# Kernel optimization log

Measured on AMD Instinct MI355X. Metric: run time of the kernel, lower is better.

Reference implementation:

```python
import jax, jax.numpy as jnp
import numpy as np

T, I, H, O = 4096, 1024, 2048, 512


def setup_inputs() -> dict:
    key = jax.random.key(0)
    ks = jax.random.split(key, 7)
    s = 1.0 / np.sqrt(H)
    return {
        "input_seq": jax.random.normal(ks[0], (T, I), dtype=jnp.float32),
        "W_ih": jax.random.uniform(ks[1], (4 * H, I), jnp.float32, -s, s),
        "W_hh": jax.random.uniform(ks[2], (4 * H, H), jnp.float32, -s, s),
        "b_ih": jax.random.uniform(ks[3], (4 * H,), jnp.float32, -s, s),
        "b_hh": jax.random.uniform(ks[4], (4 * H,), jnp.float32, -s, s),
        "W_lin": jax.random.uniform(ks[5], (O, H), jnp.float32, -s, s),
        "b_lin": jax.random.uniform(ks[6], (O,), jnp.float32, -s, s),
    }


def reference(input_seq, W_ih, W_hh, b_ih, b_hh, W_lin, b_lin):
    # Precompute input-to-gates projection for all timesteps: [T, 4H]
    x_gates = input_seq @ W_ih.T + (b_ih + b_hh)

    def step(carry, xg):
        h, c = carry  # [H], [H]
        gates = xg + W_hh @ h  # [4H]; PyTorch gate order: i, f, g, o
        i, f, g, o = jnp.split(gates, 4)
        i = jax.nn.sigmoid(i)
        f = jax.nn.sigmoid(f)
        g = jnp.tanh(g)
        o = jax.nn.sigmoid(o)
        c = f * c + i * g
        h = o * jnp.tanh(c)
        return (h, c), None

    h0 = jnp.zeros((H,), dtype=input_seq.dtype)
    c0 = jnp.zeros((H,), dtype=input_seq.dtype)
    (h_last, _), _ = jax.lax.scan(step, (h0, c0), x_gates)
    # predictions[-1] depends only on the final hidden state
    return h_last @ W_lin.T + b_lin  # [O]
```

## Files before the change

kernel.cpp:

```cpp
#include <hip/hip_runtime.h>
#include <math.h>

#define T_SEQ 4096
#define I_DIM 1024
#define H_DIM 2048
#define O_DIM 512
#define G4    8192

__global__ __launch_bounds__(256) void gemm_xg(
    const float* __restrict__ A, const float* __restrict__ W,
    const float* __restrict__ b_ih, const float* __restrict__ b_hh,
    float* __restrict__ xg)
{
  __shared__ __align__(16) float As[16][132];
  __shared__ __align__(16) float Bs[16][132];
  const int tid = threadIdx.x;
  const int t0 = blockIdx.y * 128;
  const int r0 = blockIdx.x * 128;
  const int tx = tid & 15, ty = tid >> 4;

  float acc[8][8];
  #pragma unroll
  for (int i = 0; i < 8; ++i)
    #pragma unroll
    for (int j = 0; j < 8; ++j) acc[i][j] = 0.f;

  for (int k0 = 0; k0 < I_DIM; k0 += 16) {
    #pragma unroll
    for (int i = 0; i < 2; ++i) {
      int lin = tid + i * 256;
      int row = lin >> 2;
      int kq  = (lin & 3) << 2;
      float4 va = *(const float4*)&A[(size_t)(t0 + row) * I_DIM + k0 + kq];
      As[kq+0][row] = va.x; As[kq+1][row] = va.y; As[kq+2][row] = va.z; As[kq+3][row] = va.w;
      float4 vb = *(const float4*)&W[(size_t)(r0 + row) * I_DIM + k0 + kq];
      Bs[kq+0][row] = vb.x; Bs[kq+1][row] = vb.y; Bs[kq+2][row] = vb.z; Bs[kq+3][row] = vb.w;
    }
    __syncthreads();
    #pragma unroll
    for (int kk = 0; kk < 16; ++kk) {
      float4 a0 = *(const float4*)&As[kk][ty*8];
      float4 a1 = *(const float4*)&As[kk][ty*8+4];
      float4 b0 = *(const float4*)&Bs[kk][tx*8];
      float4 b1 = *(const float4*)&Bs[kk][tx*8+4];
      float av[8] = {a0.x,a0.y,a0.z,a0.w,a1.x,a1.y,a1.z,a1.w};
      float bv[8] = {b0.x,b0.y,b0.z,b0.w,b1.x,b1.y,b1.z,b1.w};
      #pragma unroll
      for (int i = 0; i < 8; ++i)
        #pragma unroll
        for (int j = 0; j < 8; ++j)
          acc[i][j] = fmaf(av[i], bv[j], acc[i][j]);
    }
    __syncthreads();
  }

  const int rbase = r0 + tx * 8;
  const int g = rbase >> 11;
  const int q = (rbase & 2047) >> 3;
  float bias[8];
  #pragma unroll
  for (int j = 0; j < 8; ++j) bias[j] = b_ih[rbase + j] + b_hh[rbase + j];
  #pragma unroll
  for (int i = 0; i < 8; ++i) {
    int t = t0 + ty * 8 + i;
    float* dst = &xg[(size_t)t * G4 + q * 32 + g * 8];
    float4 o0 = make_float4(acc[i][0]+bias[0], acc[i][1]+bias[1], acc[i][2]+bias[2], acc[i][3]+bias[3]);
    float4 o1 = make_float4(acc[i][4]+bias[4], acc[i][5]+bias[5], acc[i][6]+bias[6], acc[i][7]+bias[7]);
    *(float4*)&dst[0] = o0;
    *(float4*)&dst[4] = o1;
  }
}

__device__ __forceinline__ float sigf(float x) {
  return 1.f / (1.f + __expf(-x));
}
__device__ __forceinline__ float tanh_fast(float x) {
  return 1.f - 2.f / (__expf(2.f * x) + 1.f);
}

__global__ __launch_bounds__(512, 2) void lstm_seq(
    const float* __restrict__ W_hh, const float* __restrict__ xg,
    uint2* __restrict__ hbuf )
{
  __shared__ __align__(16) float smem[21000];
  float* hsh = smem;

  const int tid  = threadIdx.x;
  const int b    = blockIdx.x;
  const int lane = tid & 63;
  const int w    = tid >> 6;

  float4 wt[4][8];
  #pragma unroll
  for (int g = 0; g < 4; ++g) {
    const float* wr = &W_hh[(size_t)(g * H_DIM + 8 * b + w) * H_DIM + 4 * lane];
    #pragma unroll
    for (int k = 0; k < 8; ++k) wt[g][k] = *(const float4*)&wr[256 * k];
  }

  float c_reg = 0.f;
  bool gaveup = false;

  const float* xp0 = &xg[(size_t)0 * G4 + b * 32 + w];
  float xgi = xp0[0], xgf = xp0[8], xgg = xp0[16], xgo = xp0[24];

  for (int t = 0; t < T_SEQ; ++t) {
    const uint2* hb = hbuf + ((t & 1) << 11);
    const unsigned tag = (unsigned)t;

    const uint2* a0 = hb + 256 * w + 4 * lane;
    uint4 f0, f1;
    int tries = 0;
    for (;;) {
      asm volatile("global_load_dwordx4 %0, %2, off sc0 sc1\n\t"
                   "global_load_dwordx4 %1, %3, off sc0 sc1\n\t"
                   "s_waitcnt vmcnt(0)"
                   : "=&v"(f0), "=&v"(f1)
                   : "v"(a0), "v"(a0 + 2)
                   : "memory");
      bool ok = (f0.y == tag) & (f0.w == tag) & (f1.y == tag) & (f1.w == tag);
      if (__all(ok) || gaveup) break;
      if (++tries > (1 << 17)) { gaveup = true; break; }
    }

    float* hd = hsh + ((t & 1) << 11);
    float4 hv4 = make_float4(__uint_as_float(f0.x), __uint_as_float(f0.z),
                             __uint_as_float(f1.x), __uint_as_float(f1.z));
    *(float4*)&hd[256 * w + 4 * lane] = hv4;

    float nxi = 0.f, nxf = 0.f, nxg = 0.f, nxo = 0.f;
    if (t + 1 < T_SEQ) {
      const float* xp = &xg[(size_t)(t + 1) * G4 + b * 32 + w];
      nxi = xp[0]; nxf = xp[8]; nxg = xp[16]; nxo = xp[24];
    }

    __syncthreads();

    float s0 = 0.f, s1 = 0.f, s2 = 0.f, s3 = 0.f;
    #pragma unroll
    for (int k = 0; k < 8; ++k) {
      float4 hv = *(const float4*)&hd[4 * lane + 256 * k];
      s0 = fmaf(wt[0][k].x, hv.x, s0); s0 = fmaf(wt[0][k].y, hv.y, s0);
      s0 = fmaf(wt[0][k].z, hv.z, s0); s0 = fmaf(wt[0][k].w, hv.w, s0);
      s1 = fmaf(wt[1][k].x, hv.x, s1); s1 = fmaf(wt[1][k].y, hv.y, s1);
      s1 = fmaf(wt[1][k].z, hv.z, s1); s1 = fmaf(wt[1][k].w, hv.w, s1);
      s2 = fmaf(wt[2][k].x, hv.x, s2); s2 = fmaf(wt[2][k].y, hv.y, s2);
      s2 = fmaf(wt[2][k].z, hv.z, s2); s2 = fmaf(wt[2][k].w, hv.w, s2);
      s3 = fmaf(wt[3][k].x, hv.x, s3); s3 = fmaf(wt[3][k].y, hv.y, s3);
      s3 = fmaf(wt[3][k].z, hv.z, s3); s3 = fmaf(wt[3][k].w, hv.w, s3);
    }

    #pragma unroll
    for (int sh = 32; sh >= 1; sh >>= 1) {
      s0 += __shfl_xor(s0, sh, 64);
      s1 += __shfl_xor(s1, sh, 64);
      s2 += __shfl_xor(s2, sh, 64);
      s3 += __shfl_xor(s3, sh, 64);
    }

    if (lane == 0) {
      float iv = sigf(s0 + xgi);
      float fv = sigf(s1 + xgf);
      float gv = tanh_fast(s2 + xgg);
      float ov = sigf(s3 + xgo);
      c_reg = fv * c_reg + iv * gv;
      float hv = ov * tanh_fast(c_reg);
      uint2 pv;
      pv.x = __float_as_uint(hv);
      pv.y = (unsigned)(t + 1);
      uint2* dst = hbuf + (((t + 1) & 1) << 11) + 8 * b + w;
      asm volatile("global_store_dwordx2 %0, %1, off sc0 sc1"
                   :: "v"(dst), "v"(pv) : "memory");
    }

    xgi = nxi; xgf = nxf; xgg = nxg; xgo = nxo;
  }
}

__global__ __launch_bounds__(256) void proj_out(
    const float* __restrict__ W_lin, const float* __restrict__ b_lin,
    const uint2* __restrict__ hpairs, float* __restrict__ out)
{
  const int tid = threadIdx.x;
  const int lane = tid & 63;
  const int w4 = tid >> 6;
  const int o = blockIdx.x * 4 + w4;
  const float* wr = &W_lin[(size_t)o * H_DIM + 4 * lane];
  float s = 0.f;
  #pragma unroll
  for (int k = 0; k < 8; ++k) {
    float4 wv = *(const float4*)&wr[256 * k];
    uint4 p0 = *(const uint4*)&hpairs[4 * lane + 256 * k];
    uint4 p1 = *(const uint4*)&hpairs[4 * lane + 256 * k + 2];
    s = fmaf(wv.x, __uint_as_float(p0.x), s);
    s = fmaf(wv.y, __uint_as_float(p0.z), s);
    s = fmaf(wv.z, __uint_as_float(p1.x), s);
    s = fmaf(wv.w, __uint_as_float(p1.z), s);
  }
  #pragma unroll
  for (int sh = 32; sh >= 1; sh >>= 1) s += __shfl_xor(s, sh, 64);
  if (lane == 0) out[o] = s + b_lin[o];
}

extern "C" void kernel_launch(void* const* d_in, const int* in_sizes, int n_in,
                              void* d_out, int out_size, void* d_ws, size_t ws_size,
                              hipStream_t stream)
{
  const float* input = (const float*)d_in[0];
  const float* W_ih  = (const float*)d_in[1];
  const float* W_hh  = (const float*)d_in[2];
  const float* b_ih  = (const float*)d_in[3];
  const float* b_hh  = (const float*)d_in[4];
  const float* W_lin = (const float*)d_in[5];
  const float* b_lin = (const float*)d_in[6];
  float* out = (float*)d_out;

  char* ws = (char*)d_ws;
  const size_t XG_BYTES = (size_t)T_SEQ * G4 * sizeof(float);
  float* xg   = (float*)ws;
  uint2* hbuf = (uint2*)(ws + XG_BYTES);

  hipMemsetAsync(ws + XG_BYTES, 0, 2 * H_DIM * sizeof(uint2), stream);

  gemm_xg<<<dim3(64, 32), 256, 0, stream>>>(input, W_ih, b_ih, b_hh, xg);
  lstm_seq<<<256, 512, 0, stream>>>(W_hh, xg, hbuf);
  proj_out<<<128, 256, 0, stream>>>(W_lin, b_lin, hbuf, out);
}
```

Baseline: 13.07 ms.

## Relay hidden state through per-XCC gateway block mailboxes for L2-local polling

For each XCC, the first block to arrive becomes a gateway. It polls the global h buffer with system-coherent loads and copies what it reads into a mailbox buffer owned by that XCC. The other blocks poll the mailbox with sc0-only loads that can hit the shared L2, and fall back to the LLC path after many failed tries. The aim is to cut cross-die coherent polling traffic and latency in the per-step grid-wide synchronization. The cost is an extra relay hop through the gateway, and correctness relies on non-coherent L2 visibility of the gateway's plain stores.

```diff
diff --git a/kernel.cpp b/kernel.cpp
--- a/kernel.cpp
+++ b/kernel.cpp
@@ -80,16 +80,32 @@
 
 __global__ __launch_bounds__(512, 2) void lstm_seq(
     const float* __restrict__ W_hh, const float* __restrict__ xg,
-    uint2* __restrict__ hbuf )
+    uint2* __restrict__ hbuf ,
+    uint2* __restrict__ mail ,
+    int*   __restrict__ gwcnt )
 {
   __shared__ __align__(16) float smem[21000];
   float* hsh = smem;
+  __shared__ int s_gw;
+  __shared__ int s_xcc;
 
   const int tid  = threadIdx.x;
   const int b    = blockIdx.x;
   const int lane = tid & 63;
   const int w    = tid >> 6;
 
+  if (tid == 0) {
+    unsigned xcc;
+    asm volatile("s_getreg_b32 %0, hwreg(HW_REG_XCC_ID, 0, 32)" : "=s"(xcc));
+    xcc &= 7;
+    s_xcc = (int)xcc;
+    s_gw  = (atomicAdd(&gwcnt[xcc], 1) == 0) ? 1 : 0;
+  }
+  __syncthreads();
+  const int  xcc   = s_xcc;
+  const bool is_gw = (s_gw != 0);
+  uint2* mb_base = mail + (xcc << 12);
+
   float4 wt[4][8];
   #pragma unroll
   for (int g = 0; g < 4; ++g) {
@@ -100,30 +116,61 @@
 
   float c_reg = 0.f;
   bool gaveup = false;
+  bool use_llc = false;
 
   const float* xp0 = &xg[(size_t)0 * G4 + b * 32 + w];
   float xgi = xp0[0], xgf = xp0[8], xgg = xp0[16], xgo = xp0[24];
 
   for (int t = 0; t < T_SEQ; ++t) {
-    const uint2* hb = hbuf + ((t & 1) << 11);
+    const int par = t & 1;
     const unsigned tag = (unsigned)t;
-
-    const uint2* a0 = hb + 256 * w + 4 * lane;
+    const uint2* ha = hbuf + (par << 11) + 256 * w + 4 * lane;
+    uint2*       ma = mb_base + (par << 11) + 256 * w + 4 * lane;
+
     uint4 f0, f1;
-    int tries = 0;
-    for (;;) {
-      asm volatile("global_load_dwordx4 %0, %2, off sc0 sc1\n\t"
-                   "global_load_dwordx4 %1, %3, off sc0 sc1\n\t"
-                   "s_waitcnt vmcnt(0)"
-                   : "=&v"(f0), "=&v"(f1)
-                   : "v"(a0), "v"(a0 + 2)
-                   : "memory");
-      bool ok = (f0.y == tag) & (f0.w == tag) & (f1.y == tag) & (f1.w == tag);
-      if (__all(ok) || gaveup) break;
-      if (++tries > (1 << 17)) { gaveup = true; break; }
-    }
-
-    float* hd = hsh + ((t & 1) << 11);
+    if (is_gw) {
+      int tries = 0;
+      for (;;) {
+        asm volatile("global_load_dwordx4 %0, %2, off sc0 sc1\n\t"
+                     "global_load_dwordx4 %1, %3, off sc0 sc1\n\t"
+                     "s_waitcnt vmcnt(0)"
+                     : "=&v"(f0), "=&v"(f1)
+                     : "v"(ha), "v"(ha + 2)
+                     : "memory");
+        bool ok = (f0.y == tag) & (f0.w == tag) & (f1.y == tag) & (f1.w == tag);
+        if (__all(ok) || gaveup) break;
+        if (++tries > (1 << 20)) { gaveup = true; break; }
+      }
+      ((uint4*)ma)[0] = f0;
+      ((uint4*)ma)[1] = f1;
+    } else {
+      int tries = 0;
+      for (;;) {
+        if (!use_llc) {
+          asm volatile("global_load_dwordx4 %0, %2, off sc0\n\t"
+                       "global_load_dwordx4 %1, %3, off sc0\n\t"
+                       "s_waitcnt vmcnt(0)"
+                       : "=&v"(f0), "=&v"(f1)
+                       : "v"(ma), "v"(ma + 2)
+                       : "memory");
+          bool ok = (f0.y == tag) & (f0.w == tag) & (f1.y == tag) & (f1.w == tag);
+          if (__all(ok) || gaveup) break;
+          if (++tries > (1 << 14)) { use_llc = true; tries = 0; }
+        } else {
+          asm volatile("global_load_dwordx4 %0, %2, off sc0 sc1\n\t"
+                       "global_load_dwordx4 %1, %3, off sc0 sc1\n\t"
+                       "s_waitcnt vmcnt(0)"
+                       : "=&v"(f0), "=&v"(f1)
+                       : "v"(ha), "v"(ha + 2)
+                       : "memory");
+          bool ok = (f0.y == tag) & (f0.w == tag) & (f1.y == tag) & (f1.w == tag);
+          if (__all(ok) || gaveup) break;
+          if (++tries > (1 << 20)) { gaveup = true; break; }
+        }
+      }
+    }
+
+    float* hd = hsh + (par << 11);
     float4 hv4 = make_float4(__uint_as_float(f0.x), __uint_as_float(f0.z),
                              __uint_as_float(f1.x), __uint_as_float(f1.z));
     *(float4*)&hd[256 * w + 4 * lane] = hv4;
@@ -216,13 +263,17 @@
   float* out = (float*)d_out;
 
   char* ws = (char*)d_ws;
-  const size_t XG_BYTES = (size_t)T_SEQ * G4 * sizeof(float);
-  float* xg   = (float*)ws;
-  uint2* hbuf = (uint2*)(ws + XG_BYTES);
-
-  hipMemsetAsync(ws + XG_BYTES, 0, 2 * H_DIM * sizeof(uint2), stream);
+  const size_t XG_BYTES   = (size_t)T_SEQ * G4 * sizeof(float);
+  const size_t HB_BYTES   = 2ull * H_DIM * sizeof(uint2);
+  const size_t MAIL_BYTES = 8ull * 2 * H_DIM * sizeof(uint2);
+  float* xg    = (float*)ws;
+  uint2* hbuf  = (uint2*)(ws + XG_BYTES);
+  uint2* mail  = (uint2*)(ws + XG_BYTES + HB_BYTES);
+  int*   gwcnt = (int*)  (ws + XG_BYTES + HB_BYTES + MAIL_BYTES);
+
+  (void)hipMemsetAsync(ws + XG_BYTES, 0, HB_BYTES + MAIL_BYTES + 8 * sizeof(int), stream);
 
   gemm_xg<<<dim3(64, 32), 256, 0, stream>>>(input, W_ih, b_ih, b_hh, xg);
-  lstm_seq<<<256, 512, 0, stream>>>(W_hh, xg, hbuf);
+  lstm_seq<<<256, 512, 0, stream>>>(W_hh, xg, hbuf, mail, gwcnt);
   proj_out<<<128, 256, 0, stream>>>(W_lin, b_lin, hbuf, out);
 }
```

Result: slower. 16.83 ms (+28.8%).
